# Performance work log

Measured on AMD Instinct MI355X. Metric: run time of the kernel, lower is better.

Reference implementation:

```python
import jax, jax.numpy as jnp
import numpy as np

N, D, O, E = 8192, 1024, 1024, 16

def setup_inputs() -> dict:
    key = jax.random.key(0)
    k1, k2, k3, k4 = jax.random.split(key, 4)
    scale = 1.0 / np.sqrt(D)
    x = jax.random.normal(k1, (N, D), dtype=jnp.float32)
    Wg = jax.random.normal(k2, (E, D), dtype=jnp.float32) * scale
    We = jax.random.normal(k3, (E, O, D), dtype=jnp.float32) * scale
    be = jax.random.normal(k4, (E, O), dtype=jnp.float32) * scale
    return {"x": x, "Wg": Wg, "We": We, "be": be}

def reference(x, Wg, We, be):
    # gate: softmax over experts
    gate_logits = jnp.einsum('nd,ed->ne', x, Wg)          # [N, E]
    gate_weights = jax.nn.softmax(gate_logits, axis=1)    # [N, E]
    # top-1 mask via >= max (ties keep all maxima, matching torch code)
    max_w = jnp.max(gate_weights, axis=1, keepdims=True)
    mask = (gate_weights >= max_w).astype(gate_weights.dtype)
    sw = gate_weights * mask                              # selected weights [N, E]
    # weighted sum of all-expert Linear outputs, fused (no [N,E,O] intermediate)
    out = jnp.einsum('nd,eod,ne->no', x, We, sw) + sw @ be  # [N, O]
    return (out, gate_weights)
```

## Files before the change

### kernel.cpp

```cpp
#include <hip/hip_runtime.h>
#include <hip/hip_bf16.h>

#define NROWS 8192
#define DIM   1024
#define OUTD  1024
#define NE    16
#define BM    128
#define BN    128
#define BK    32
#define MAXT  96
#define NKSTEP (DIM / BK)
#define NTILE  (OUTD / BN)

typedef short s16x8 __attribute__((ext_vector_type(8)));
typedef float f32x4 __attribute__((ext_vector_type(4)));

__device__ __forceinline__ unsigned f2bf(float f) {
  __hip_bfloat16 h = __float2bfloat16(f);
  return (unsigned)__builtin_bit_cast(unsigned short, h);
}

__device__ __forceinline__ void gload_lds16(const void* g, void* l) {
  __builtin_amdgcn_global_load_lds(
      (const __attribute__((address_space(1))) void*)g,
      (__attribute__((address_space(3))) void*)l, 16, 0, 0);
}

__global__ void init_kernel(int* counts) {
  int t = threadIdx.x;
  if (t < 32) counts[t] = 0;
}

__global__ __launch_bounds__(256) void convert_we_kernel(
    const float* __restrict__ W, ushort* __restrict__ o) {
  size_t i = ((size_t)blockIdx.x * 256 + threadIdx.x) * 8;
  float4 a = *(const float4*)(W + i);
  float4 b = *(const float4*)(W + i + 4);
  unsigned w0 = f2bf(a.x) | (f2bf(a.y) << 16);
  unsigned w1 = f2bf(a.z) | (f2bf(a.w) << 16);
  unsigned w2 = f2bf(b.x) | (f2bf(b.y) << 16);
  unsigned w3 = f2bf(b.z) | (f2bf(b.w) << 16);
  *(uint4*)(o + i) = make_uint4(w0, w1, w2, w3);
}

__global__ __launch_bounds__(256) void gate_kernel(
    const float* __restrict__ x, const float* __restrict__ Wg,
    float* __restrict__ gate_out, int* __restrict__ eid,
    float* __restrict__ wsel, ushort* __restrict__ xb,
    int* __restrict__ counts)
{
  __shared__ __align__(16) float4 wg4[NE * 256];
  __shared__ int hist[NE];
  int t = threadIdx.x, wid = t >> 6, lane = t & 63;
  if (t < NE) hist[t] = 0;
  const float4* wgg = (const float4*)Wg;
  #pragma unroll
  for (int i = 0; i < 16; ++i) wg4[t + i * 256] = wgg[t + i * 256];
  __syncthreads();

  int n0 = blockIdx.x * 16 + wid * 4;

  float acc[4][NE];
  #pragma unroll
  for (int r = 0; r < 4; ++r)
    #pragma unroll
    for (int e = 0; e < NE; ++e) acc[r][e] = 0.f;

  #pragma unroll
  for (int j = 0; j < 4; ++j) {
    float4 xv[4];
    #pragma unroll
    for (int r = 0; r < 4; ++r) {
      xv[r] = *(const float4*)(x + (size_t)(n0 + r) * DIM + j * 256 + 4 * lane);
      unsigned lo = f2bf(xv[r].x) | (f2bf(xv[r].y) << 16);
      unsigned hi = f2bf(xv[r].z) | (f2bf(xv[r].w) << 16);
      *(uint2*)(xb + (size_t)(n0 + r) * DIM + j * 256 + 4 * lane) = make_uint2(lo, hi);
    }
    #pragma unroll
    for (int e = 0; e < NE; ++e) {
      float4 w = wg4[e * 256 + j * 64 + lane];
      #pragma unroll
      for (int r = 0; r < 4; ++r)
        acc[r][e] += xv[r].x * w.x + xv[r].y * w.y + xv[r].z * w.z + xv[r].w * w.w;
    }
  }

  #pragma unroll
  for (int r = 0; r < 4; ++r) {
    int n = n0 + r;
    float v[NE];
    #pragma unroll
    for (int e = 0; e < NE; ++e) v[e] = acc[r][e];
    #pragma unroll
    for (int i = 0; i < 8; ++i) {
      float send = (lane & 32) ? v[i] : v[i + 8];
      float recv = __shfl_xor(send, 32, 64);
      v[i] = ((lane & 32) ? v[i + 8] : v[i]) + recv;
    }
    #pragma unroll
    for (int i = 0; i < 4; ++i) {
      float send = (lane & 16) ? v[i] : v[i + 4];
      float recv = __shfl_xor(send, 16, 64);
      v[i] = ((lane & 16) ? v[i + 4] : v[i]) + recv;
    }
    #pragma unroll
    for (int i = 0; i < 2; ++i) {
      float send = (lane & 8) ? v[i] : v[i + 2];
      float recv = __shfl_xor(send, 8, 64);
      v[i] = ((lane & 8) ? v[i + 2] : v[i]) + recv;
    }
    {
      float send = (lane & 4) ? v[0] : v[1];
      float recv = __shfl_xor(send, 4, 64);
      v[0] = ((lane & 4) ? v[1] : v[0]) + recv;
    }
    v[0] += __shfl_xor(v[0], 2, 64);
    v[0] += __shfl_xor(v[0], 1, 64);
    float lg = v[0];
    int e = ((lane >> 5) & 1) * 8 + ((lane >> 4) & 1) * 4 +
            ((lane >> 3) & 1) * 2 + ((lane >> 2) & 1);
    float m = lg;
    m = fmaxf(m, __shfl_xor(m, 4, 64));
    m = fmaxf(m, __shfl_xor(m, 8, 64));
    m = fmaxf(m, __shfl_xor(m, 16, 64));
    m = fmaxf(m, __shfl_xor(m, 32, 64));
    float p = expf(lg - m);
    float s = p;
    s += __shfl_xor(s, 4, 64);
    s += __shfl_xor(s, 8, 64);
    s += __shfl_xor(s, 16, 64);
    s += __shfl_xor(s, 32, 64);
    float inv = 1.f / s;
    if ((lane & 3) == 0) gate_out[(size_t)n * NE + e] = p * inv;
    unsigned long long msk = __ballot(lg == m);
    if (lane == 0) {
      int fl = __builtin_ctzll(msk);
      int ebest = ((fl >> 5) & 1) * 8 + ((fl >> 4) & 1) * 4 +
                  ((fl >> 3) & 1) * 2 + ((fl >> 2) & 1);
      eid[n] = ebest;
      wsel[n] = inv;
      atomicAdd(&hist[ebest], 1);
    }
  }
  __syncthreads();
  if (t < NE && hist[t]) atomicAdd(&counts[t], hist[t]);
}

__global__ void plan_kernel(const int* __restrict__ counts,
                            int* __restrict__ offsets, int4* __restrict__ tiles)
{
  int lane = threadIdx.x;
  int c = (lane < NE) ? counts[lane] : 0;
  int nt = (c + BM - 1) >> 7;
  int po = c, pt = nt;
  #pragma unroll
  for (int d = 1; d < 16; d <<= 1) {
    int oc = __shfl_up(po, d, 64);
    int ot = __shfl_up(pt, d, 64);
    if (lane >= d) { po += oc; pt += ot; }
  }
  int off = po - c;
  int tbase = pt - nt;
  if (lane < NE) offsets[lane] = off;
  if (lane == NE - 1) offsets[NE] = po;
  int total_t = __shfl(pt, NE - 1, 64);
  if (lane < NE) {
    int ti = 0;
    for (int m = 0; m < c; m += BM, ++ti)
      tiles[tbase + ti] = make_int4(lane, off + m, (c - m < BM) ? (c - m) : BM, 0);
  }
  for (int i = total_t + lane; i < MAXT; i += 64)
    tiles[i] = make_int4(-1, 0, 0, 0);
}

__global__ __launch_bounds__(256) void scatter_kernel(
    const int* __restrict__ eid, const int* __restrict__ offsets,
    int* __restrict__ cursors, int* __restrict__ rowids)
{
  __shared__ int h[NE];
  __shared__ int base[NE];
  int t = threadIdx.x;
  if (t < NE) h[t] = 0;
  __syncthreads();
  int n = blockIdx.x * 256 + t;
  int e = eid[n];
  int local = atomicAdd(&h[e], 1);
  __syncthreads();
  if (t < NE) base[t] = h[t] ? atomicAdd(&cursors[t], h[t]) : 0;
  __syncthreads();
  rowids[offsets[e] + base[e] + local] = n;
}

__global__ __launch_bounds__(256) void moe_gemm_kernel(
    const ushort* __restrict__ xb, const ushort* __restrict__ Web,
    const float* __restrict__ be, const int* __restrict__ rowids,
    const float* __restrict__ wsel, const int4* __restrict__ tiles,
    float* __restrict__ out)
{
  __shared__ __align__(16) char lds[32768];
  __shared__ int   rows_s[BM];
  __shared__ float w_s[BM];

  int4 ti = tiles[blockIdx.x];
  int e = ti.x;
  if (e < 0) return;
  int srow = ti.y, nvalid = ti.z;
  int t = threadIdx.x, lane = t & 63;
  int wid = t >> 6, wm = wid >> 1, wn = wid & 1;
  int ncol0 = blockIdx.y * BN;

  if (t < BM) {
    int valid = t < nvalid;
    int rid = valid ? rowids[srow + t] : 0;
    rows_s[t] = valid ? rid : -1;
    w_s[t] = valid ? wsel[rid] : 0.f;
  }

  int r1 = t >> 2, sl = t & 3;
  int r2 = r1 + 64;
  int cg = sl ^ ((r1 >> 1) & 3);
  int rida1 = (r1 < nvalid) ? rowids[srow + r1] : 0;
  int rida2 = (r2 < nvalid) ? rowids[srow + r2] : 0;
  const ushort* ap1 = xb + (size_t)rida1 * DIM + cg * 8;
  const ushort* ap2 = xb + (size_t)rida2 * DIM + cg * 8;
  const ushort* bb  = Web + (size_t)e * OUTD * DIM + (size_t)ncol0 * DIM + cg * 8;
  const ushort* bp1 = bb + (size_t)r1 * DIM;
  const ushort* bp2 = bb + (size_t)r2 * DIM;

  f32x4 zero = {0.f, 0.f, 0.f, 0.f};
  f32x4 acc[4][4];
  #pragma unroll
  for (int i = 0; i < 4; ++i)
    #pragma unroll
    for (int j = 0; j < 4; ++j) acc[i][j] = zero;

  auto stage = [&](int b, int koff) {
    char* A = lds + b * 8192;
    char* B = lds + 16384 + b * 8192;
    gload_lds16(ap1 + koff, A + t * 16);
    gload_lds16(ap2 + koff, A + 4096 + t * 16);
    gload_lds16(bp1 + koff, B + t * 16);
    gload_lds16(bp2 + koff, B + 4096 + t * 16);
  };
  stage(0, 0);

  unsigned rl15 = lane & 15, rcg = lane >> 4;
  for (int ks = 0; ks < NKSTEP; ++ks) {
    __syncthreads();
    if (ks + 1 < NKSTEP) stage((ks + 1) & 1, (ks + 1) * BK);
    const char* A = lds + (ks & 1) * 8192;
    const char* B = lds + 16384 + (ks & 1) * 8192;
    s16x8 af[4], bf_[4];
    #pragma unroll
    for (int f = 0; f < 4; ++f) {
      unsigned rA = wm * 64 + f * 16 + rl15;
      af[f] = *(const s16x8*)(A + rA * 64 + ((rcg ^ ((rA >> 1) & 3)) * 16));
      unsigned rB = wn * 64 + f * 16 + rl15;
      bf_[f] = *(const s16x8*)(B + rB * 64 + ((rcg ^ ((rB >> 1) & 3)) * 16));
    }
    #pragma unroll
    for (int fm = 0; fm < 4; ++fm)
      #pragma unroll
      for (int fn = 0; fn < 4; ++fn)
        acc[fm][fn] = __builtin_amdgcn_mfma_f32_16x16x32_bf16(af[fm], bf_[fn], acc[fm][fn], 0, 0, 0);
  }

  int rgrp = lane >> 4;
  #pragma unroll
  for (int fn = 0; fn < 4; ++fn) {
    int col = ncol0 + wn * 64 + fn * 16 + (lane & 15);
    float bev = be[e * OUTD + col];
    #pragma unroll
    for (int fm = 0; fm < 4; ++fm) {
      #pragma unroll
      for (int j = 0; j < 4; ++j) {
        int rl = wm * 64 + fm * 16 + rgrp * 4 + j;
        int orow = rows_s[rl];
        if (orow >= 0) {
          float w = w_s[rl];
          out[(size_t)orow * OUTD + col] = w * (acc[fm][fn][j] + bev);
        }
      }
    }
  }
}

extern "C" void kernel_launch(void* const* d_in, const int* in_sizes, int n_in,
                              void* d_out, int out_size, void* d_ws, size_t ws_size,
                              hipStream_t stream) {
  const float* x  = (const float*)d_in[0];
  const float* Wg = (const float*)d_in[1];
  const float* We = (const float*)d_in[2];
  const float* be = (const float*)d_in[3];
  float* out = (float*)d_out;
  float* gate_out = out + (size_t)NROWS * OUTD;

  char* ws = (char*)d_ws;
  int*  counts  = (int*)ws;
  int*  cursors = counts + 16;
  int*  offsets = counts + 32;
  int4* tiles   = (int4*)(ws + 256);
  int*  eidp    = (int*)(ws + 4096);
  float* wselp  = (float*)(ws + 4096 + 4 * NROWS);
  int*  rowids  = (int*)(ws + 4096 + 8 * NROWS);
  ushort* xb    = (ushort*)(ws + (1u << 20));
  ushort* Web   = (ushort*)(ws + (1u << 20) + 16777216u);

  hipLaunchKernelGGL(init_kernel, dim3(1), dim3(64), 0, stream, counts);
  hipLaunchKernelGGL(convert_we_kernel, dim3(8192), dim3(256), 0, stream, We, Web);
  hipLaunchKernelGGL(gate_kernel, dim3(NROWS / 16), dim3(256), 0, stream,
                     x, Wg, gate_out, eidp, wselp, xb, counts);
  hipLaunchKernelGGL(plan_kernel, dim3(1), dim3(64), 0, stream, counts, offsets, tiles);
  hipLaunchKernelGGL(scatter_kernel, dim3(NROWS / 256), dim3(256), 0, stream,
                     eidp, offsets, cursors, rowids);
  hipLaunchKernelGGL(moe_gemm_kernel, dim3(MAXT, NTILE), dim3(256), 0, stream,
                     xb, Web, be, rowids, wselp, tiles, out);
}
```

Before: 221.8 us.

## Fuse gate and weight conversion, drop init kernel, triple-buffer narrower GEMM tiles

```diff
diff --git a/kernel.cpp b/kernel.cpp
--- a/kernel.cpp
+++ b/kernel.cpp
@@ -6,11 +6,13 @@
 #define OUTD  1024
 #define NE    16
 #define BM    128
-#define BN    128
+#define BN    64
 #define BK    32
 #define MAXT  96
 #define NKSTEP (DIM / BK)
 #define NTILE  (OUTD / BN)
+#define GATEBLKS 512
+#define CONVBLKS 2048
 
 typedef short s16x8 __attribute__((ext_vector_type(8)));
 typedef float f32x4 __attribute__((ext_vector_type(4)));
@@ -26,32 +28,35 @@
       (__attribute__((address_space(3))) void*)l, 16, 0, 0);
 }
 
-__global__ void init_kernel(int* counts) {
-  int t = threadIdx.x;
-  if (t < 32) counts[t] = 0;
-}
-
-__global__ __launch_bounds__(256) void convert_we_kernel(
-    const float* __restrict__ W, ushort* __restrict__ o) {
-  size_t i = ((size_t)blockIdx.x * 256 + threadIdx.x) * 8;
-  float4 a = *(const float4*)(W + i);
-  float4 b = *(const float4*)(W + i + 4);
-  unsigned w0 = f2bf(a.x) | (f2bf(a.y) << 16);
-  unsigned w1 = f2bf(a.z) | (f2bf(a.w) << 16);
-  unsigned w2 = f2bf(b.x) | (f2bf(b.y) << 16);
-  unsigned w3 = f2bf(b.z) | (f2bf(b.w) << 16);
-  *(uint4*)(o + i) = make_uint4(w0, w1, w2, w3);
-}
-
-__global__ __launch_bounds__(256) void gate_kernel(
+__global__ __launch_bounds__(256) void gate_conv_kernel(
     const float* __restrict__ x, const float* __restrict__ Wg,
+    const float* __restrict__ We,
     float* __restrict__ gate_out, int* __restrict__ eid,
     float* __restrict__ wsel, ushort* __restrict__ xb,
-    int* __restrict__ counts)
+    ushort* __restrict__ Web, int* __restrict__ hist_g)
 {
   __shared__ __align__(16) float4 wg4[NE * 256];
   __shared__ int hist[NE];
-  int t = threadIdx.x, wid = t >> 6, lane = t & 63;
+  int t = threadIdx.x;
+
+  if (blockIdx.x >= GATEBLKS) {
+    int b = blockIdx.x - GATEBLKS;
+    size_t base = ((size_t)b * 256 + t) * 8;
+    #pragma unroll
+    for (int i = 0; i < 4; ++i) {
+      size_t idx = base + (size_t)i * ((size_t)CONVBLKS * 256 * 8);
+      float4 a = *(const float4*)(We + idx);
+      float4 c = *(const float4*)(We + idx + 4);
+      unsigned w0 = f2bf(a.x) | (f2bf(a.y) << 16);
+      unsigned w1 = f2bf(a.z) | (f2bf(a.w) << 16);
+      unsigned w2 = f2bf(c.x) | (f2bf(c.y) << 16);
+      unsigned w3 = f2bf(c.z) | (f2bf(c.w) << 16);
+      *(uint4*)(Web + idx) = make_uint4(w0, w1, w2, w3);
+    }
+    return;
+  }
+
+  int wid = t >> 6, lane = t & 63;
   if (t < NE) hist[t] = 0;
   const float4* wgg = (const float4*)Wg;
   #pragma unroll
@@ -143,39 +148,54 @@
     }
   }
   __syncthreads();
-  if (t < NE && hist[t]) atomicAdd(&counts[t], hist[t]);
-}
-
-__global__ void plan_kernel(const int* __restrict__ counts,
-                            int* __restrict__ offsets, int4* __restrict__ tiles)
+  if (t < NE) hist_g[blockIdx.x * NE + t] = hist[t];
+}
+
+__global__ __launch_bounds__(256) void plan_kernel(
+    const int* __restrict__ hist_g, int* __restrict__ offsets,
+    int* __restrict__ cursors, int4* __restrict__ tiles)
 {
-  int lane = threadIdx.x;
-  int c = (lane < NE) ? counts[lane] : 0;
-  int nt = (c + BM - 1) >> 7;
-  int po = c, pt = nt;
-  #pragma unroll
-  for (int d = 1; d < 16; d <<= 1) {
-    int oc = __shfl_up(po, d, 64);
-    int ot = __shfl_up(pt, d, 64);
-    if (lane >= d) { po += oc; pt += ot; }
-  }
-  int off = po - c;
-  int tbase = pt - nt;
-  if (lane < NE) offsets[lane] = off;
-  if (lane == NE - 1) offsets[NE] = po;
-  int total_t = __shfl(pt, NE - 1, 64);
-  if (lane < NE) {
-    int ti = 0;
-    for (int m = 0; m < c; m += BM, ++ti)
-      tiles[tbase + ti] = make_int4(lane, off + m, (c - m < BM) ? (c - m) : BM, 0);
-  }
-  for (int i = total_t + lane; i < MAXT; i += 64)
+  __shared__ int part[16][17];
+  __shared__ int sh_total;
+  int t = threadIdx.x;
+  int e = t & 15, chunk = t >> 4;
+  int s = 0;
+  #pragma unroll
+  for (int i = 0; i < 32; ++i) s += hist_g[(chunk * 32 + i) * NE + e];
+  part[chunk][e] = s;
+  __syncthreads();
+  if (t < 64) {
+    int lane = t;
+    int c = 0;
+    if (lane < NE) {
+      #pragma unroll
+      for (int ch = 0; ch < 16; ++ch) c += part[ch][lane];
+    }
+    int nt = (c + BM - 1) >> 7;
+    int po = c, pt = nt;
+    #pragma unroll
+    for (int d = 1; d < 16; d <<= 1) {
+      int oc = __shfl_up(po, d, 64);
+      int ot = __shfl_up(pt, d, 64);
+      if (lane >= d) { po += oc; pt += ot; }
+    }
+    int off = po - c, tbase = pt - nt;
+    if (lane < NE) { offsets[lane] = off; cursors[lane] = off; }
+    if (lane == NE - 1) { offsets[NE] = po; sh_total = pt; }
+    if (lane < NE) {
+      int ti = 0;
+      for (int m = 0; m < c; m += BM, ++ti)
+        tiles[tbase + ti] = make_int4(lane, off + m, (c - m < BM) ? (c - m) : BM, 0);
+    }
+  }
+  __syncthreads();
+  for (int i = sh_total + t; i < MAXT; i += 256)
     tiles[i] = make_int4(-1, 0, 0, 0);
 }
 
 __global__ __launch_bounds__(256) void scatter_kernel(
-    const int* __restrict__ eid, const int* __restrict__ offsets,
-    int* __restrict__ cursors, int* __restrict__ rowids)
+    const int* __restrict__ eid, int* __restrict__ cursors,
+    int* __restrict__ rowids)
 {
   __shared__ int h[NE];
   __shared__ int base[NE];
@@ -188,16 +208,16 @@
   __syncthreads();
   if (t < NE) base[t] = h[t] ? atomicAdd(&cursors[t], h[t]) : 0;
   __syncthreads();
-  rowids[offsets[e] + base[e] + local] = n;
-}
-
-__global__ __launch_bounds__(256) void moe_gemm_kernel(
+  rowids[base[e] + local] = n;
+}
+
+__global__ __launch_bounds__(256, 4) void moe_gemm_kernel(
     const ushort* __restrict__ xb, const ushort* __restrict__ Web,
     const float* __restrict__ be, const int* __restrict__ rowids,
     const float* __restrict__ wsel, const int4* __restrict__ tiles,
     float* __restrict__ out)
 {
-  __shared__ __align__(16) char lds[32768];
+  __shared__ __align__(16) char lds[3 * 12288];
   __shared__ int   rows_s[BM];
   __shared__ float w_s[BM];
 
@@ -223,52 +243,70 @@
   int rida2 = (r2 < nvalid) ? rowids[srow + r2] : 0;
   const ushort* ap1 = xb + (size_t)rida1 * DIM + cg * 8;
   const ushort* ap2 = xb + (size_t)rida2 * DIM + cg * 8;
-  const ushort* bb  = Web + (size_t)e * OUTD * DIM + (size_t)ncol0 * DIM + cg * 8;
-  const ushort* bp1 = bb + (size_t)r1 * DIM;
-  const ushort* bp2 = bb + (size_t)r2 * DIM;
+  const ushort* bp1 = Web + (size_t)e * OUTD * DIM + (size_t)(ncol0 + r1) * DIM + cg * 8;
 
   f32x4 zero = {0.f, 0.f, 0.f, 0.f};
-  f32x4 acc[4][4];
+  f32x4 acc[4][2];
   #pragma unroll
   for (int i = 0; i < 4; ++i)
     #pragma unroll
-    for (int j = 0; j < 4; ++j) acc[i][j] = zero;
-
-  auto stage = [&](int b, int koff) {
-    char* A = lds + b * 8192;
-    char* B = lds + 16384 + b * 8192;
+    for (int j = 0; j < 2; ++j) acc[i][j] = zero;
+
+  auto stage = [&](int bufoff, int koff) {
+    char* A = lds + bufoff;
+    char* B = A + 8192;
     gload_lds16(ap1 + koff, A + t * 16);
     gload_lds16(ap2 + koff, A + 4096 + t * 16);
     gload_lds16(bp1 + koff, B + t * 16);
-    gload_lds16(bp2 + koff, B + 4096 + t * 16);
   };
-  stage(0, 0);
 
   unsigned rl15 = lane & 15, rcg = lane >> 4;
-  for (int ks = 0; ks < NKSTEP; ++ks) {
-    __syncthreads();
-    if (ks + 1 < NKSTEP) stage((ks + 1) & 1, (ks + 1) * BK);
-    const char* A = lds + (ks & 1) * 8192;
-    const char* B = lds + 16384 + (ks & 1) * 8192;
-    s16x8 af[4], bf_[4];
+  auto body = [&](int bufoff) {
+    const char* A = lds + bufoff;
+    const char* B = A + 8192;
+    s16x8 af[4], bf_[2];
     #pragma unroll
     for (int f = 0; f < 4; ++f) {
       unsigned rA = wm * 64 + f * 16 + rl15;
       af[f] = *(const s16x8*)(A + rA * 64 + ((rcg ^ ((rA >> 1) & 3)) * 16));
-      unsigned rB = wn * 64 + f * 16 + rl15;
+    }
+    #pragma unroll
+    for (int f = 0; f < 2; ++f) {
+      unsigned rB = wn * 32 + f * 16 + rl15;
       bf_[f] = *(const s16x8*)(B + rB * 64 + ((rcg ^ ((rB >> 1) & 3)) * 16));
     }
     #pragma unroll
     for (int fm = 0; fm < 4; ++fm)
       #pragma unroll
-      for (int fn = 0; fn < 4; ++fn)
+      for (int fn = 0; fn < 2; ++fn)
         acc[fm][fn] = __builtin_amdgcn_mfma_f32_16x16x32_bf16(af[fm], bf_[fn], acc[fm][fn], 0, 0, 0);
-  }
+  };
+
+  asm volatile("s_waitcnt vmcnt(0)" ::: "memory");
+  stage(0, 0);
+  stage(12288, BK);
+  int stg = 24576, cur = 0;
+
+  for (int ks = 0; ks < NKSTEP - 1; ++ks) {
+    asm volatile("s_waitcnt vmcnt(3)" ::: "memory");
+    __builtin_amdgcn_s_barrier();
+    asm volatile("" ::: "memory");
+    if (ks < NKSTEP - 2) {
+      stage(stg, (ks + 2) * BK);
+      stg = (stg == 24576) ? 0 : stg + 12288;
+    }
+    body(cur);
+    cur = (cur == 24576) ? 0 : cur + 12288;
+  }
+  asm volatile("s_waitcnt vmcnt(0)" ::: "memory");
+  __builtin_amdgcn_s_barrier();
+  asm volatile("" ::: "memory");
+  body(cur);
 
   int rgrp = lane >> 4;
   #pragma unroll
-  for (int fn = 0; fn < 4; ++fn) {
-    int col = ncol0 + wn * 64 + fn * 16 + (lane & 15);
+  for (int fn = 0; fn < 2; ++fn) {
+    int col = ncol0 + wn * 32 + fn * 16 + (lane & 15);
     float bev = be[e * OUTD + col];
     #pragma unroll
     for (int fm = 0; fm < 4; ++fm) {
@@ -296,23 +334,22 @@
   float* gate_out = out + (size_t)NROWS * OUTD;
 
   char* ws = (char*)d_ws;
-  int*  counts  = (int*)ws;
-  int*  cursors = counts + 16;
-  int*  offsets = counts + 32;
+  int*  cursors = (int*)ws;
+  int*  offsets = (int*)(ws + 64);
   int4* tiles   = (int4*)(ws + 256);
-  int*  eidp    = (int*)(ws + 4096);
-  float* wselp  = (float*)(ws + 4096 + 4 * NROWS);
-  int*  rowids  = (int*)(ws + 4096 + 8 * NROWS);
+  int*  hist_g  = (int*)(ws + 4096);
+  int*  eidp    = (int*)(ws + 40960);
+  float* wselp  = (float*)(ws + 40960 + 4 * NROWS);
+  int*  rowids  = (int*)(ws + 40960 + 8 * NROWS);
   ushort* xb    = (ushort*)(ws + (1u << 20));
   ushort* Web   = (ushort*)(ws + (1u << 20) + 16777216u);
 
-  hipLaunchKernelGGL(init_kernel, dim3(1), dim3(64), 0, stream, counts);
-  hipLaunchKernelGGL(convert_we_kernel, dim3(8192), dim3(256), 0, stream, We, Web);
-  hipLaunchKernelGGL(gate_kernel, dim3(NROWS / 16), dim3(256), 0, stream,
-                     x, Wg, gate_out, eidp, wselp, xb, counts);
-  hipLaunchKernelGGL(plan_kernel, dim3(1), dim3(64), 0, stream, counts, offsets, tiles);
+  hipLaunchKernelGGL(gate_conv_kernel, dim3(GATEBLKS + CONVBLKS), dim3(256), 0, stream,
+                     x, Wg, We, gate_out, eidp, wselp, xb, Web, hist_g);
+  hipLaunchKernelGGL(plan_kernel, dim3(1), dim3(256), 0, stream,
+                     hist_g, offsets, cursors, tiles);
   hipLaunchKernelGGL(scatter_kernel, dim3(NROWS / 256), dim3(256), 0, stream,
-                     eidp, offsets, cursors, rowids);
+                     eidp, cursors, rowids);
   hipLaunchKernelGGL(moe_gemm_kernel, dim3(MAXT, NTILE), dim3(256), 0, stream,
                      xb, Web, be, rowids, wselp, tiles, out);
 }
```

Result: slower. 231.6 us (+4.4%).
